# Optimization experiments

Measured on AMD Instinct MI355X. Metric: run time of the kernel, lower is better.

The kernel has to match this reference:

```python
import jax, jax.numpy as jnp
import numpy as np

SQRT_D = 16.0   # sqrt(d), d=256
BETA2 = 18.0    # beta^2 / 2, beta=6
EPS_BN = 1e-5


def _bn1d(x, g, b):
    # eval-mode BatchNorm1d with freshly-initialized running stats (mean=0, var=1)
    scale = g / jnp.sqrt(1.0 + EPS_BN)
    if x.ndim == 3:  # [B, C, N]
        return x * scale[:, None] + b[:, None]
    return x * scale + b  # [B, C]


def _crelu(z):
    return jax.nn.relu(z.real) + 1j * jax.nn.relu(z.imag)


def _sa_layer(x, qk_w, v_w, v_b, t_w, t_b, g, b):
    # x: [B, C, N]; q and k share weights (q_conv.weight = k_conv.weight)
    xq = jnp.einsum('oc,bcn->bno', qk_w, x)            # [B, N, C/4]
    xk = jnp.einsum('oc,bcn->bon', qk_w, x)            # [B, C/4, N]
    xv = jnp.einsum('oc,bcn->bon', v_w, x) + v_b[:, None]
    energy = jnp.einsum('bno,bom->bnm', xq, xk)        # [B, N, N]
    att = jax.nn.softmax(energy, axis=-1)
    att = att / (1e-9 + att.sum(axis=1, keepdims=True))  # sum-normalized over dim=1
    xr = jnp.einsum('bcn,bnm->bcm', xv, att)           # [B, C, N]
    xr = jax.nn.relu(_bn1d(jnp.einsum('oc,bcn->bon', t_w, x - xr) + t_b[:, None], g, b))
    return x + xr


def _forward(x, A, P, cl1_wr, cl1_wi, cl1_br, cl1_bi, cl2_wr, cl2_wi, cl2_br, cl2_bi,
             pt_conv1_w, pt_conv2_w, pt_bn1_g, pt_bn1_b, pt_bn2_g, pt_bn2_b,
             sa_qk_w, sa_v_w, sa_v_b, sa_t_w, sa_t_b, sa_bn_g, sa_bn_b,
             fuse_w, fuse_bn_g, fuse_bn_b, lin1_w, bn6_g, bn6_b,
             lin2_w, lin2_b, bn7_g, bn7_b, lin3_w, lin3_b):
    pts = jnp.transpose(x, (0, 2, 1))                  # [B, N, 3]
    # ---- VecKM: pairwise Gaussian kernel times complex random features ----
    sq = jnp.sum(pts * pts, axis=-1)                   # [B, N]
    D2 = sq[:, :, None] + sq[:, None, :] - 2.0 * jnp.einsum('bnc,bmc->bnm', pts, pts)
    J = jnp.exp(-BETA2 * D2).astype(jnp.complex64)     # [B, N, N]
    eA = jnp.exp(1j * (pts @ A))                       # [B, N, d] complex64
    G = (J @ eA) / eA
    G = G / jnp.linalg.norm(G, axis=-1, keepdims=True) * SQRT_D
    G = G + jnp.exp(1j * (pts @ P))                    # positional encoding
    # ---- ComplexLinear -> ComplexReLU -> ComplexLinear ----
    W1 = (cl1_wr + 1j * cl1_wi).astype(jnp.complex64)
    G = _crelu(G @ W1.T + (cl1_br + 1j * cl1_bi))
    W2 = (cl2_wr + 1j * cl2_wi).astype(jnp.complex64)
    G = G @ W2.T + (cl2_br + 1j * cl2_bi)
    Gr = G.real ** 2 + G.imag ** 2                     # [B, N, 256]
    Gc = jnp.transpose(Gr, (0, 2, 1))                  # [B, 256, N]
    # ---- Point_Transformer_Last ----
    h = jax.nn.relu(_bn1d(jnp.einsum('oc,bcn->bon', pt_conv1_w, Gc), pt_bn1_g, pt_bn1_b))
    h = jax.nn.relu(_bn1d(jnp.einsum('oc,bcn->bon', pt_conv2_w, h), pt_bn2_g, pt_bn2_b))
    feats = []
    for i in range(4):
        h = _sa_layer(h, sa_qk_w[i], sa_v_w[i], sa_v_b[i], sa_t_w[i], sa_t_b[i],
                      sa_bn_g[i], sa_bn_b[i])
        feats.append(h)
    h = jnp.concatenate(feats + [Gc], axis=1)          # [B, 1280, N]
    h = jax.nn.leaky_relu(_bn1d(jnp.einsum('oc,bcn->bon', fuse_w, h), fuse_bn_g, fuse_bn_b), 0.2)
    h = jnp.max(h, axis=-1)                            # adaptive_max_pool1d -> [B, 1024]
    h = jax.nn.leaky_relu(_bn1d(h @ lin1_w.T, bn6_g, bn6_b), 0.2)
    h = jax.nn.leaky_relu(_bn1d(h @ lin2_w.T + lin2_b, bn7_g, bn7_b), 0.2)
    return h @ lin3_w.T + lin3_b                       # [B, 40]


def setup_inputs() -> dict:
    key = jax.random.key(0)
    ks = iter(jax.random.split(key, 64))
    B, N, d = 16, 1024, 256
    r = lambda shape, s=0.05: jax.random.normal(next(ks), shape, dtype=jnp.float32) * s
    inp = {
        'x': jax.random.normal(next(ks), (B, 3, N), dtype=jnp.float32),
        'A': jax.random.normal(next(ks), (3, d), dtype=jnp.float32) * 30.0,
        'P': jax.random.normal(next(ks), (3, d), dtype=jnp.float32),
        'cl1_wr': r((d, d)), 'cl1_wi': r((d, d)), 'cl1_br': r((d,)), 'cl1_bi': r((d,)),
        'cl2_wr': r((d, d)), 'cl2_wi': r((d, d)), 'cl2_br': r((d,)), 'cl2_bi': r((d,)),
        'pt_conv1_w': r((256, 256)), 'pt_conv2_w': r((256, 256)),
        'pt_bn1_g': jnp.ones(256), 'pt_bn1_b': jnp.zeros(256),
        'pt_bn2_g': jnp.ones(256), 'pt_bn2_b': jnp.zeros(256),
        'sa_qk_w': r((4, 64, 256)), 'sa_v_w': r((4, 256, 256)), 'sa_v_b': r((4, 256)),
        'sa_t_w': r((4, 256, 256)), 'sa_t_b': r((4, 256)),
        'sa_bn_g': jnp.ones((4, 256)), 'sa_bn_b': jnp.zeros((4, 256)),
        'fuse_w': r((1024, 1280)), 'fuse_bn_g': jnp.ones(1024), 'fuse_bn_b': jnp.zeros(1024),
        'lin1_w': r((512, 1024)), 'bn6_g': jnp.ones(512), 'bn6_b': jnp.zeros(512),
        'lin2_w': r((256, 512)), 'lin2_b': r((256,)),
        'bn7_g': jnp.ones(256), 'bn7_b': jnp.zeros(256),
        'lin3_w': r((40, 256)), 'lin3_b': r((40,)),
    }
    return inp


def reference(x, A, P, cl1_wr, cl1_wi, cl1_br, cl1_bi, cl2_wr, cl2_wi, cl2_br, cl2_bi,
              pt_conv1_w, pt_conv2_w, pt_bn1_g, pt_bn1_b, pt_bn2_g, pt_bn2_b,
              sa_qk_w, sa_v_w, sa_v_b, sa_t_w, sa_t_b, sa_bn_g, sa_bn_b,
              fuse_w, fuse_bn_g, fuse_bn_b, lin1_w, bn6_g, bn6_b,
              lin2_w, lin2_b, bn7_g, bn7_b, lin3_w, lin3_b):
    return _forward(x, A, P, cl1_wr, cl1_wi, cl1_br, cl1_bi, cl2_wr, cl2_wi, cl2_br, cl2_bi,
                    pt_conv1_w, pt_conv2_w, pt_bn1_g, pt_bn1_b, pt_bn2_g, pt_bn2_b,
                    sa_qk_w, sa_v_w, sa_v_b, sa_t_w, sa_t_b, sa_bn_g, sa_bn_b,
                    fuse_w, fuse_bn_g, fuse_bn_b, lin1_w, bn6_g, bn6_b,
                    lin2_w, lin2_b, bn7_g, bn7_b, lin3_w, lin3_b)
```

## Files before the change

kernel.cpp:

```cpp
#include <hip/hip_runtime.h>
#include <math.h>

#define BB 16
#define NN 1024
#define DD 256

typedef unsigned short u16;
typedef unsigned int uint32;
typedef __attribute__((ext_vector_type(8))) short s8v;
typedef __attribute__((ext_vector_type(4))) float f4v;

__device__ __forceinline__ u16 f2b(float f) {
  uint32 u = __float_as_uint(f);
  return (u16)((u + 0x7fffu + ((u >> 16) & 1u)) >> 16);
}
__device__ __forceinline__ float b2f(u16 u) {
  return __uint_as_float(((uint32)u) << 16);
}

__device__ __forceinline__ float waveRedSum(float v) {
  #pragma unroll
  for (int o = 32; o; o >>= 1) v += __shfl_xor(v, o, 64);
  return v;
}
__device__ __forceinline__ float waveRedMax(float v) {
  #pragma unroll
  for (int o = 32; o; o >>= 1) v = fmaxf(v, __shfl_xor(v, o, 64));
  return v;
}

__global__ void k_pts(const float* __restrict__ x, float* __restrict__ pts) {
  int i = blockIdx.x * 256 + threadIdx.x;
  if (i >= BB * NN) return;
  int b = i >> 10, n = i & 1023;
  const float* xb = x + (size_t)b * 3 * NN;
  pts[i * 3 + 0] = xb[n];
  pts[i * 3 + 1] = xb[NN + n];
  pts[i * 3 + 2] = xb[2 * NN + n];
}

__global__ void k_phase(const float* __restrict__ pts, const float* __restrict__ A,
                        float2* __restrict__ eA) {
  int i = blockIdx.x * 256 + threadIdx.x;
  int d = i & 255; int bn = i >> 8;
  float p0 = pts[bn * 3], p1 = pts[bn * 3 + 1], p2 = pts[bn * 3 + 2];
  float ta = p0 * A[d] + p1 * A[256 + d] + p2 * A[512 + d];
  float s, c;
  sincosf(ta, &s, &c); eA[i] = make_float2(c, s);
}

__global__ void k_eat(const float2* __restrict__ eA, u16* __restrict__ eAT) {
  int bid = blockIdx.x;
  int dt = bid & 7, nt = (bid >> 3) & 15, b = bid >> 7;
  int d0 = dt * 32, n0 = nt * 64;
  __shared__ u16 cosT[32][72], sinT[32][72];
  int t = threadIdx.x;
  {
    int n = t >> 2, dg = (t & 3) * 8;
    const float2* p = eA + ((size_t)(b * 1024 + n0 + n)) * 256 + d0 + dg;
    #pragma unroll
    for (int j = 0; j < 8; j++) {
      float2 v = p[j];
      cosT[dg + j][n] = f2b(v.x);
      sinT[dg + j][n] = f2b(v.y);
    }
  }
  __syncthreads();
  {
    int rr = t >> 2, ng = (t & 3) * 16;
    int d = rr >> 1, cmp = rr & 1;
    const u16* src = (cmp ? &sinT[d][ng] : &cosT[d][ng]);
    uint4 v0 = *(const uint4*)src;
    uint4 v1 = *(const uint4*)(src + 8);
    u16* dst = eAT + ((size_t)(b * 512 + 2 * d0 + rr)) * 1024 + n0 + ng;
    *(uint4*)dst = v0;
    *(uint4*)(dst + 8) = v1;
  }
}

__global__ void k_jbuild(const float* __restrict__ pts, u16* __restrict__ J) {
  int bid = blockIdx.x;
  int b = bid >> 10, n = bid & 1023;
  int t = threadIdx.x;
  const float* pb = pts + (size_t)b * 3072;
  float pnx = pb[n * 3], pny = pb[n * 3 + 1], pnz = pb[n * 3 + 2];
  int m = t * 4;
  const float* pm = pb + (size_t)m * 3;
  float4 a = *(const float4*)pm;
  float4 bq = *(const float4*)(pm + 4);
  float4 c = *(const float4*)(pm + 8);
  float dx, dy, dz, d2;
  dx = a.x - pnx;  dy = a.y - pny;  dz = a.z - pnz;  d2 = dx*dx + dy*dy + dz*dz;
  float j0 = __expf(-18.0f * d2);
  dx = a.w - pnx;  dy = bq.x - pny; dz = bq.y - pnz; d2 = dx*dx + dy*dy + dz*dz;
  float j1 = __expf(-18.0f * d2);
  dx = bq.z - pnx; dy = bq.w - pny; dz = c.x - pnz;  d2 = dx*dx + dy*dy + dz*dz;
  float j2 = __expf(-18.0f * d2);
  dx = c.y - pnx;  dy = c.z - pny;  dz = c.w - pnz;  d2 = dx*dx + dy*dy + dz*dz;
  float j3 = __expf(-18.0f * d2);
  uint32 lo = (uint32)f2b(j0) | ((uint32)f2b(j1) << 16);
  uint32 hi = (uint32)f2b(j2) | ((uint32)f2b(j3) << 16);
  *(uint2*)(J + (size_t)bid * 1024 + m) = make_uint2(lo, hi);
}

__global__ void k_norm(const float2* __restrict__ M, const float2* __restrict__ eA,
                       const float* __restrict__ pts, const float* __restrict__ P,
                       u16* __restrict__ Gb) {
  int bn = blockIdx.x; int c = threadIdx.x;
  size_t idx = (size_t)bn * DD + c;
  float2 m = M[idx], e = eA[idx];
  float gr = m.x * e.x + m.y * e.y;
  float gi = m.y * e.x - m.x * e.y;
  float s = gr * gr + gi * gi;
  s = waveRedSum(s);
  __shared__ float red[4];
  if ((c & 63) == 0) red[c >> 6] = s;
  __syncthreads();
  float tot = red[0] + red[1] + red[2] + red[3];
  float scale = 16.0f / sqrtf(tot);
  float p0 = pts[bn * 3], p1 = pts[bn * 3 + 1], p2 = pts[bn * 3 + 2];
  float tp = p0 * P[c] + p1 * P[256 + c] + p2 * P[512 + c];
  float sp, cp; sincosf(tp, &sp, &cp);
  uint32 pk = (uint32)f2b(gr * scale + cp) | ((uint32)f2b(gi * scale + sp) << 16);
  *(uint32*)(Gb + idx * 2) = pk;
}

__global__ void k_cast(const float* __restrict__ s, u16* __restrict__ d, int n) {
  int i = blockIdx.x * 256 + threadIdx.x;
  if (i < n) d[i] = f2b(s[i]);
}
__global__ void k_wprep(const float* __restrict__ wr, const float* __restrict__ wi,
                        u16* __restrict__ dst) {
  int i = blockIdx.x * 256 + threadIdx.x;
  int op = i >> 9, c2 = i & 511, c = c2 >> 1, pl = c2 & 1;
  float v;
  if (op < 256) v = pl ? -wi[op * 256 + c] : wr[op * 256 + c];
  else          v = pl ?  wr[(op - 256) * 256 + c] : wi[(op - 256) * 256 + c];
  dst[i] = f2b(v);
}
__global__ void k_cbias(const float* __restrict__ br, const float* __restrict__ bi,
                        float* __restrict__ cb) {
  int t = threadIdx.x;
  cb[t] = (t < 256) ? br[t] : bi[t - 256];
}

__global__ void k_g2(const u16* __restrict__ G2b, u16* __restrict__ bigT) {
  int i = blockIdx.x * 256 + threadIdx.x;
  int row = i >> 8, c = i & 255;
  float re = b2f(G2b[(size_t)row * 512 + 2 * c]);
  float im = b2f(G2b[(size_t)row * 512 + 2 * c + 1]);
  bigT[(size_t)row * 1280 + 1024 + c] = f2b(re * re + im * im);
}

template<int BM>
__launch_bounds__(256)
__global__ void k_mm(const u16* __restrict__ Ab, long a_bs, int lda,
                     const u16* __restrict__ Btb, long b_bs, int ldb,
                     int K, int tiles_m, int tiles_n,
                     const float* __restrict__ bias,
                     const float* __restrict__ bng, const float* __restrict__ bnb,
                     const float* __restrict__ cbias,
                     int act,
                     const float* __restrict__ res, long res_bs, int res_sub,
                     float* __restrict__ outF, long outF_bs, int ldF,
                     u16* __restrict__ outB, long outB_bs, int ldBo, int ileave,
                     u16* __restrict__ outT, long outT_bs, int ldT) {
  constexpr int BN = 128;
  constexpr int WM = (BM == 128) ? 64 : 32;
  constexpr int MI = WM / 16;
  __shared__ u16 smem[BN * BM];
  u16* As = smem;
  u16* Bs = smem + BM * 32;
  int t = threadIdx.x;
  int l = t & 63, w = t >> 6;
  int p = l & 15, q = l >> 4;
  int bid = blockIdx.x;
  int tn = bid % tiles_n;
  int tm = (bid / tiles_n) % tiles_m;
  int b  = bid / (tiles_n * tiles_m);
  int m0 = tm * BM, n0 = tn * BN;
  int wm = w >> 1, wn = w & 1;
  const u16* Ap = Ab + (size_t)b * a_bs;
  const u16* Bp = Btb + (size_t)b * b_bs;

  f4v acc[MI][4];
  #pragma unroll
  for (int i = 0; i < MI; i++)
    #pragma unroll
    for (int j = 0; j < 4; j++) acc[i][j] = (f4v){0.f, 0.f, 0.f, 0.f};

  int arow = t >> 2, kg = (t & 3) * 8;
  for (int k0 = 0; k0 < K; k0 += 32) {
    __syncthreads();
    #pragma unroll
    for (int it = 0; it < BM / 64; it++) {
      int r = it * 64 + arow;
      float4 v = *(const float4*)(Ap + (size_t)(m0 + r) * lda + k0 + kg);
      *(float4*)&As[r * 32 + kg] = v;
    }
    #pragma unroll
    for (int it = 0; it < 2; it++) {
      int r = it * 64 + arow;
      float4 v = *(const float4*)(Bp + (size_t)(n0 + r) * ldb + k0 + kg);
      *(float4*)&Bs[r * 32 + kg] = v;
    }
    __syncthreads();
    s8v af[MI], bf[4];
    #pragma unroll
    for (int i = 0; i < MI; i++)
      af[i] = *(const s8v*)&As[(wm * WM + i * 16 + p) * 32 + q * 8];
    #pragma unroll
    for (int j = 0; j < 4; j++)
      bf[j] = *(const s8v*)&Bs[(wn * 64 + j * 16 + p) * 32 + q * 8];
    #pragma unroll
    for (int i = 0; i < MI; i++)
      #pragma unroll
      for (int j = 0; j < 4; j++)
        acc[i][j] = __builtin_amdgcn_mfma_f32_16x16x32_bf16(af[i], bf[j], acc[i][j], 0, 0, 0);
  }

  __syncthreads();

  float cbv[4];
  #pragma unroll
  for (int j = 0; j < 4; j++) {
    int no = n0 + wn * 64 + j * 16 + p;
    cbv[j] = cbias ? cbias[no] : 0.0f;
  }
  const float BNS = 0.99999500003749966f;
  #pragma unroll
  for (int i = 0; i < MI; i++) {
    #pragma unroll
    for (int r = 0; r < 4; r++) {
      int mo = m0 + wm * WM + i * 16 + q * 4 + r;
      float mult = 1.f, add = 0.f;
      if (bias) add = bias[mo];
      if (bng) { float s = bng[mo] * BNS; add = add * s + bnb[mo]; mult = s; }
      #pragma unroll
      for (int j = 0; j < 4; j++) {
        int no = n0 + wn * 64 + j * 16 + p;
        float v = acc[i][j][r];
        v = v * mult + add;
        if (cbias) v += cbv[j];
        if (act == 1) v = fmaxf(v, 0.f);
        else if (act == 2) v = v > 0.f ? v : 0.2f * v;
        if (res) {
          float rv = res[(size_t)b * res_bs + (size_t)mo * NN + no];
          v = res_sub ? rv - v : rv + v;
        }
        if (outF) outF[(size_t)b * outF_bs + (size_t)mo * ldF + no] = v;
        if (outB) {
          int noo = ileave ? (((no & 255) << 1) | (no >> 8)) : no;
          outB[(size_t)b * outB_bs + (size_t)mo * ldBo + noo] = f2b(v);
        }
        if (outT) smem[(wn * 64 + j * 16 + p) * BM + (mo - m0)] = f2b(v);
      }
    }
  }
  if (outT) {
    __syncthreads();
    constexpr int CPR = BM / 8;
    constexpr int RPP = 256 / CPR;
    int row0 = t / CPR, cg = (t % CPR) * 8;
    for (int rr = row0; rr < BN; rr += RPP) {
      float4 v = *(const float4*)&smem[rr * BM + cg];
      *(float4*)(outT + (size_t)b * outT_bs + (size_t)(n0 + rr) * ldT + m0 + cg) = v;
    }
  }
}

__global__ void k_rowstats(const float* __restrict__ E, float* __restrict__ rmax_,
                           float* __restrict__ rinv_) {
  int row = blockIdx.x;
  const float* pp = E + (size_t)row * NN;
  int t = threadIdx.x;
  float4 v = *(const float4*)(pp + t * 4);
  float mx = fmaxf(fmaxf(v.x, v.y), fmaxf(v.z, v.w));
  mx = waveRedMax(mx);
  __shared__ float redm[4];
  __shared__ float reds[4];
  if ((t & 63) == 0) redm[t >> 6] = mx;
  __syncthreads();
  mx = fmaxf(fmaxf(redm[0], redm[1]), fmaxf(redm[2], redm[3]));
  float s = __expf(v.x - mx) + __expf(v.y - mx) + __expf(v.z - mx) + __expf(v.w - mx);
  s = waveRedSum(s);
  if ((t & 63) == 0) reds[t >> 6] = s;
  __syncthreads();
  if (t == 0) {
    float tot = reds[0] + reds[1] + reds[2] + reds[3];
    rmax_[row] = mx;
    rinv_[row] = 1.0f / tot;
  }
}

__launch_bounds__(256)
__global__ void k_xratt(const u16* __restrict__ xv_, const float* __restrict__ E,
                        const float* __restrict__ rmax_, const float* __restrict__ rinv_,
                        const float* __restrict__ XinF, long xinF_bs,
                        u16* __restrict__ diffT) {
  __shared__ u16 smem[16384];
  __shared__ float colred[128][4];
  u16* As = smem;
  u16* Bs = smem + 4096;
  int t = threadIdx.x;
  int l = t & 63, w = t >> 6;
  int p = l & 15, q = l >> 4;
  int bid = blockIdx.x;
  int mt = bid & 7, ct = (bid >> 3) & 1, b = bid >> 4;
  int c0 = ct * 128, m0 = mt * 128;
  int wm = w >> 1, wn = w & 1;
  const u16* Ap = xv_ + (size_t)b * 262144;
  const float* Ep = E + ((size_t)b << 20);
  const float* rmx = rmax_ + (b << 10);
  const float* riv = rinv_ + (b << 10);
  f4v acc[4][4];
  #pragma unroll
  for (int i = 0; i < 4; i++)
    #pragma unroll
    for (int j = 0; j < 4; j++) acc[i][j] = (f4v){0.f, 0.f, 0.f, 0.f};
  float colpart0 = 0.f, colpart1 = 0.f;
  int arow = t >> 2, kg = (t & 3) * 8;
  for (int k0 = 0; k0 < 1024; k0 += 32) {
    __syncthreads();
    #pragma unroll
    for (int it = 0; it < 2; it++) {
      int r = it * 64 + arow;
      *(float4*)&As[r * 32 + kg] = *(const float4*)(Ap + (size_t)(c0 + r) * 1024 + k0 + kg);
    }
    float4 ma0 = *(const float4*)(rmx + k0 + kg);
    float4 ma1 = *(const float4*)(rmx + k0 + kg + 4);
    float4 ia0 = *(const float4*)(riv + k0 + kg);
    float4 ia1 = *(const float4*)(riv + k0 + kg + 4);
    #pragma unroll
    for (int it = 0; it < 2; it++) {
      int r = it * 64 + arow;
      const float* ep = Ep + (size_t)(m0 + r) * 1024 + k0 + kg;
      float4 e0 = *(const float4*)ep;
      float4 e1 = *(const float4*)(ep + 4);
      float p0 = __expf(e0.x - ma0.x) * ia0.x;
      float p1 = __expf(e0.y - ma0.y) * ia0.y;
      float p2 = __expf(e0.z - ma0.z) * ia0.z;
      float p3 = __expf(e0.w - ma0.w) * ia0.w;
      float p4 = __expf(e1.x - ma1.x) * ia1.x;
      float p5 = __expf(e1.y - ma1.y) * ia1.y;
      float p6 = __expf(e1.z - ma1.z) * ia1.z;
      float p7 = __expf(e1.w - ma1.w) * ia1.w;
      float s8 = ((p0 + p1) + (p2 + p3)) + ((p4 + p5) + (p6 + p7));
      if (it == 0) colpart0 += s8; else colpart1 += s8;
      uint32 w0 = (uint32)f2b(p0) | ((uint32)f2b(p1) << 16);
      uint32 w1 = (uint32)f2b(p2) | ((uint32)f2b(p3) << 16);
      uint32 w2 = (uint32)f2b(p4) | ((uint32)f2b(p5) << 16);
      uint32 w3 = (uint32)f2b(p6) | ((uint32)f2b(p7) << 16);
      *(uint4*)&Bs[r * 32 + kg] = make_uint4(w0, w1, w2, w3);
    }
    __syncthreads();
    s8v af[4], bf[4];
    #pragma unroll
    for (int i = 0; i < 4; i++)
      af[i] = *(const s8v*)&As[(wm * 64 + i * 16 + p) * 32 + q * 8];
    #pragma unroll
    for (int j = 0; j < 4; j++)
      bf[j] = *(const s8v*)&Bs[(wn * 64 + j * 16 + p) * 32 + q * 8];
    #pragma unroll
    for (int i = 0; i < 4; i++)
      #pragma unroll
      for (int j = 0; j < 4; j++)
        acc[i][j] = __builtin_amdgcn_mfma_f32_16x16x32_bf16(af[i], bf[j], acc[i][j], 0, 0, 0);
  }
  colred[arow][t & 3] = colpart0;
  colred[64 + arow][t & 3] = colpart1;
  __syncthreads();
  float csv[4];
  #pragma unroll
  for (int j = 0; j < 4; j++) {
    int ml = wn * 64 + j * 16 + p;
    csv[j] = 1.0f / (1e-9f + colred[ml][0] + colred[ml][1] + colred[ml][2] + colred[ml][3]);
  }
  #pragma unroll
  for (int i = 0; i < 4; i++) {
    #pragma unroll
    for (int r = 0; r < 4; r++) {
      int cl = wm * 64 + i * 16 + q * 4 + r;
      int c = c0 + cl;
      #pragma unroll
      for (int j = 0; j < 4; j++) {
        int ml = wn * 64 + j * 16 + p;
        float v = acc[i][j][r] * csv[j];
        float rv = XinF[(size_t)b * xinF_bs + (size_t)c * 1024 + m0 + ml];
        smem[ml * 128 + cl] = f2b(rv - v);
      }
    }
  }
  __syncthreads();
  int rr0 = t >> 4, cg = (t & 15) * 8;
  #pragma unroll
  for (int k = 0; k < 8; k++) {
    int rr = rr0 + k * 16;
    *(float4*)(diffT + (size_t)b * 262144 + (size_t)(m0 + rr) * 256 + c0 + cg) =
        *(const float4*)&smem[rr * 128 + cg];
  }
}

__global__ void k_maxpool(const float* __restrict__ fin, float* __restrict__ pool) {
  int bo = blockIdx.x;
  const float* pp = fin + (size_t)bo * NN;
  int t = threadIdx.x;
  float m = fmaxf(fmaxf(pp[t], pp[t + 256]), fmaxf(pp[t + 512], pp[t + 768]));
  m = waveRedMax(m);
  __shared__ float red[4];
  if ((t & 63) == 0) red[t >> 6] = m;
  __syncthreads();
  if (t == 0) pool[bo] = fmaxf(fmaxf(red[0], red[1]), fmaxf(red[2], red[3]));
}

__global__ void k_fc(const float* __restrict__ in, int Cc,
                     const float* __restrict__ W,
                     const float* __restrict__ bias,
                     const float* __restrict__ bng, const float* __restrict__ bnb,
                     int act, float* __restrict__ out, int O) {
  int i = blockIdx.x * 256 + threadIdx.x;
  if (i >= BB * O) return;
  int b = i / O, o = i % O;
  const float* xp = in + (size_t)b * Cc;
  const float* wp = W + (size_t)o * Cc;
  float s = 0.f;
  for (int c = 0; c < Cc; c += 4) {
    float4 xv = *(const float4*)(xp + c);
    float4 wv = *(const float4*)(wp + c);
    s += xv.x * wv.x + xv.y * wv.y + xv.z * wv.z + xv.w * wv.w;
  }
  if (bias) s += bias[o];
  const float BNS = 0.99999500003749966f;
  if (bng) s = s * (bng[o] * BNS) + bnb[o];
  if (act == 2) s = s > 0.f ? s : 0.2f * s;
  else if (act == 1) s = fmaxf(s, 0.f);
  out[i] = s;
}

extern "C" void kernel_launch(void* const* d_in, const int* in_sizes, int n_in,
                              void* d_out, int out_size, void* d_ws, size_t ws_size,
                              hipStream_t stream) {
  const float* x        = (const float*)d_in[0];
  const float* A        = (const float*)d_in[1];
  const float* P        = (const float*)d_in[2];
  const float* cl1_wr   = (const float*)d_in[3];
  const float* cl1_wi   = (const float*)d_in[4];
  const float* cl1_br   = (const float*)d_in[5];
  const float* cl1_bi   = (const float*)d_in[6];
  const float* cl2_wr   = (const float*)d_in[7];
  const float* cl2_wi   = (const float*)d_in[8];
  const float* cl2_br   = (const float*)d_in[9];
  const float* cl2_bi   = (const float*)d_in[10];
  const float* pt_c1_w  = (const float*)d_in[11];
  const float* pt_c2_w  = (const float*)d_in[12];
  const float* pt_bn1_g = (const float*)d_in[13];
  const float* pt_bn1_b = (const float*)d_in[14];
  const float* pt_bn2_g = (const float*)d_in[15];
  const float* pt_bn2_b = (const float*)d_in[16];
  const float* sa_qk_w  = (const float*)d_in[17];
  const float* sa_v_w   = (const float*)d_in[18];
  const float* sa_v_b   = (const float*)d_in[19];
  const float* sa_t_w   = (const float*)d_in[20];
  const float* sa_t_b   = (const float*)d_in[21];
  const float* sa_bn_g  = (const float*)d_in[22];
  const float* sa_bn_b  = (const float*)d_in[23];
  const float* fuse_w   = (const float*)d_in[24];
  const float* fuse_g   = (const float*)d_in[25];
  const float* fuse_b   = (const float*)d_in[26];
  const float* lin1_w   = (const float*)d_in[27];
  const float* bn6_g    = (const float*)d_in[28];
  const float* bn6_b    = (const float*)d_in[29];
  const float* lin2_w   = (const float*)d_in[30];
  const float* lin2_b   = (const float*)d_in[31];
  const float* bn7_g    = (const float*)d_in[32];
  const float* bn7_b    = (const float*)d_in[33];
  const float* lin3_w   = (const float*)d_in[34];
  const float* lin3_b   = (const float*)d_in[35];

  float* ws = (float*)d_ws;
  const size_t oPts  = 0;
  const size_t oS    = 65536;
  const size_t oBigT = oS + 16777216;
  const size_t oXf0  = oBigT + 10485760;
  const size_t oXf1  = oXf0 + 4194304;
  const size_t oH1T  = oXf1 + 4194304;
  const size_t oH2T  = oH1T + 2097152;
  const size_t oXkT  = oH2T + 2097152;
  const size_t oXv   = oXkT + 524288;
  const size_t oAux  = oXv + 2097152;
  const size_t oGb   = oAux + 8388608;
  const size_t oW1c  = oGb + 4194304;
  const size_t oW2c  = oW1c + 131072;
  const size_t oCb1  = oW2c + 131072;
  const size_t oCb2  = oCb1 + 512;
  const size_t oPool = oCb2 + 512;
  const size_t oFc1  = oPool + 16384;
  const size_t oFc2  = oFc1 + 8192;
  const size_t oWp   = oFc2 + 4096;

  float*  pts  = ws + oPts;
  float2* eA   = (float2*)(ws + oS);
  float2* Mj   = (float2*)(ws + oS + 8388608);
  u16*    G1b  = (u16*)(ws + oS);
  u16*    G2b  = (u16*)(ws + oS + 8388608);
  float*  Ebuf = ws + oS;
  float*  fuseO= ws + oS;
  u16*    bigT = (u16*)(ws + oBigT);
  float*  Xf0  = ws + oXf0;
  float*  Xf1  = ws + oXf1;
  u16*    h1T  = (u16*)(ws + oH1T);
  u16*    diffT= (u16*)(ws + oH1T);
  u16*    h2T  = (u16*)(ws + oH2T);
  u16*    xkT  = (u16*)(ws + oXkT);
  u16*    xv   = (u16*)(ws + oXv);
  u16*    eAT  = (u16*)(ws + oAux);
  u16*    Jb   = (u16*)(ws + oAux + 4194304);
  float*  rmax = ws + oAux;
  float*  rinv = ws + oAux + 16384;
  u16*    Gb   = (u16*)(ws + oGb);
  u16*    W1c  = (u16*)(ws + oW1c);
  u16*    W2c  = (u16*)(ws + oW2c);
  float*  cb1  = ws + oCb1;
  float*  cb2  = ws + oCb2;
  float*  pool = ws + oPool;
  float*  fc1  = ws + oFc1;
  float*  fc2  = ws + oFc2;
  u16*    wp   = (u16*)(ws + oWp);
  u16* wp_pt1  = wp;
  u16* wp_pt2  = wp + 65536;
  u16* wp_qk   = wp + 131072;
  u16* wp_v    = wp + 196608;
  u16* wp_t    = wp + 458752;
  u16* wp_fuse = wp + 720896;

  k_cast<<<256, 256, 0, stream>>>(pt_c1_w, wp_pt1, 65536);
  k_cast<<<256, 256, 0, stream>>>(pt_c2_w, wp_pt2, 65536);
  k_cast<<<256, 256, 0, stream>>>(sa_qk_w, wp_qk, 65536);
  k_cast<<<1024, 256, 0, stream>>>(sa_v_w, wp_v, 262144);
  k_cast<<<1024, 256, 0, stream>>>(sa_t_w, wp_t, 262144);
  k_cast<<<5120, 256, 0, stream>>>(fuse_w, wp_fuse, 1310720);
  k_wprep<<<1024, 256, 0, stream>>>(cl1_wr, cl1_wi, W1c);
  k_wprep<<<1024, 256, 0, stream>>>(cl2_wr, cl2_wi, W2c);
  k_cbias<<<1, 512, 0, stream>>>(cl1_br, cl1_bi, cb1);
  k_cbias<<<1, 512, 0, stream>>>(cl2_br, cl2_bi, cb2);

  k_pts<<<64, 256, 0, stream>>>(x, pts);
  k_phase<<<16384, 256, 0, stream>>>(pts, A, eA);
  k_eat<<<2048, 256, 0, stream>>>(eA, eAT);
  k_jbuild<<<16384, 256, 0, stream>>>(pts, Jb);
  k_mm<128><<<512, 256, 0, stream>>>(Jb, 1048576, 1024, eAT, 524288, 1024, 1024, 8, 4,
      nullptr, nullptr, nullptr, nullptr, 0, nullptr, 0, 0,
      (float*)Mj, 524288, 512, nullptr, 0, 0, 0, nullptr, 0, 0);
  k_norm<<<BB * NN, 256, 0, stream>>>(Mj, eA, pts, P, Gb);

  k_mm<128><<<512, 256, 0, stream>>>(Gb, 0, 512, W1c, 0, 512, 512, 128, 4,
      nullptr, nullptr, nullptr, cb1, 1, nullptr, 0, 0,
      nullptr, 0, 0, G1b, 0, 512, 1, nullptr, 0, 0);
  k_mm<128><<<512, 256, 0, stream>>>(G1b, 0, 512, W2c, 0, 512, 512, 128, 4,
      nullptr, nullptr, nullptr, cb2, 0, nullptr, 0, 0,
      nullptr, 0, 0, G2b, 0, 512, 1, nullptr, 0, 0);
  k_g2<<<16384, 256, 0, stream>>>(G2b, bigT);

  const long bsBigT = 1310720;
  const long bsH256 = 262144;
  const long bsXkT  = 65536;
  const long bsXvU  = 262144;
  const long bsF    = 262144;
  const long bsE    = 1048576;

  k_mm<128><<<256, 256, 0, stream>>>(wp_pt1, 0, 256, bigT + 1024, bsBigT, 1280, 256, 2, 8,
      nullptr, pt_bn1_g, pt_bn1_b, nullptr, 1, nullptr, 0, 0,
      nullptr, 0, 0, nullptr, 0, 0, 0, h1T, bsH256, 256);
  k_mm<128><<<256, 256, 0, stream>>>(wp_pt2, 0, 256, h1T, bsH256, 256, 256, 2, 8,
      nullptr, pt_bn2_g, pt_bn2_b, nullptr, 1, nullptr, 0, 0,
      Xf0, bsF, 1024, nullptr, 0, 0, 0, h2T, bsH256, 256);

  for (int i = 0; i < 4; i++) {
    const u16* XinT   = (i == 0) ? h2T : (bigT + (i - 1) * 256);
    long       xinT_bs= (i == 0) ? bsH256 : bsBigT;
    int        xinT_ld= (i == 0) ? 256 : 1280;
    float*     XinF   = (i & 1) ? Xf1 : Xf0;
    float*     XoutF  = (i & 1) ? Xf0 : Xf1;
    const u16* qkw = wp_qk + (size_t)i * 16384;
    const u16* vw  = wp_v + (size_t)i * 65536;
    const u16* tw  = wp_t + (size_t)i * 65536;

    k_mm<64><<<128, 256, 0, stream>>>(qkw, 0, 256, XinT, xinT_bs, xinT_ld, 256, 1, 8,
        nullptr, nullptr, nullptr, nullptr, 0, nullptr, 0, 0,
        nullptr, 0, 0, nullptr, 0, 0, 0, xkT, bsXkT, 64);
    k_mm<128><<<256, 256, 0, stream>>>(vw, 0, 256, XinT, xinT_bs, xinT_ld, 256, 2, 8,
        sa_v_b + i * 256, nullptr, nullptr, nullptr, 0, nullptr, 0, 0,
        nullptr, 0, 0, xv, bsXvU, 1024, 0, nullptr, 0, 0);
    k_mm<128><<<1024, 256, 0, stream>>>(xkT, bsXkT, 64, xkT, bsXkT, 64, 64, 8, 8,
        nullptr, nullptr, nullptr, nullptr, 0, nullptr, 0, 0,
        Ebuf, bsE, 1024, nullptr, 0, 0, 0, nullptr, 0, 0);
    k_rowstats<<<BB * NN, 256, 0, stream>>>(Ebuf, rmax, rinv);
    k_xratt<<<256, 256, 0, stream>>>(xv, Ebuf, rmax, rinv, XinF, bsF, diffT);
    k_mm<128><<<256, 256, 0, stream>>>(tw, 0, 256, diffT, bsH256, 256, 256, 2, 8,
        sa_t_b + i * 256, sa_bn_g + i * 256, sa_bn_b + i * 256, nullptr, 1,
        XinF, bsF, 0,
        XoutF, bsF, 1024, nullptr, 0, 0, 0, bigT + i * 256, bsBigT, 1280);
  }

  k_mm<128><<<1024, 256, 0, stream>>>(wp_fuse, 0, 1280, bigT, bsBigT, 1280, 1280, 8, 8,
      nullptr, fuse_g, fuse_b, nullptr, 2, nullptr, 0, 0,
      fuseO, 1048576, 1024, nullptr, 0, 0, 0, nullptr, 0, 0);
  k_maxpool<<<BB * 1024, 256, 0, stream>>>(fuseO, pool);

  k_fc<<<32, 256, 0, stream>>>(pool, 1024, lin1_w, nullptr, bn6_g, bn6_b, 2, fc1, 512);
  k_fc<<<16, 256, 0, stream>>>(fc1, 512, lin2_w, lin2_b, bn7_g, bn7_b, 2, fc2, 256);
  k_fc<<<3, 256, 0, stream>>>(fc2, 256, lin3_w, lin3_b, nullptr, nullptr, 0, (float*)d_out, 40);
}
```

Baseline: 1.096 ms.

## Store attention energies in bf16 and fuse max-pool into fuse GEMM epilogue

The attention energy matrix (B×N×N) is now written as bf16 instead of fp32, which halves the traffic in the energy GEMM store, the row-stats pass and the attention-apply kernel. The fuse GEMM no longer writes its full fp32 output. It reduces per-tile row maxima in its epilogue into a small partial buffer, and a tiny kernel finishes the max over the 8 column tiles. The cost is bf16 rounding of the softmax logits, which may affect accuracy.

```diff
diff --git a/kernel.cpp b/kernel.cpp
--- a/kernel.cpp
+++ b/kernel.cpp
@@ -17,6 +17,8 @@
 __device__ __forceinline__ float b2f(u16 u) {
   return __uint_as_float(((uint32)u) << 16);
 }
+__device__ __forceinline__ float blo(uint32 w) { return __uint_as_float(w << 16); }
+__device__ __forceinline__ float bhi(uint32 w) { return __uint_as_float(w & 0xffff0000u); }
 
 __device__ __forceinline__ float waveRedSum(float v) {
   #pragma unroll
@@ -164,7 +166,8 @@
                      const float* __restrict__ res, long res_bs, int res_sub,
                      float* __restrict__ outF, long outF_bs, int ldF,
                      u16* __restrict__ outB, long outB_bs, int ldBo, int ileave,
-                     u16* __restrict__ outT, long outT_bs, int ldT) {
+                     u16* __restrict__ outT, long outT_bs, int ldT,
+                     float* __restrict__ outPool) {
   constexpr int BN = 128;
   constexpr int WM = (BM == 128) ? 64 : 32;
   constexpr int MI = WM / 16;
@@ -227,6 +230,11 @@
     int no = n0 + wn * 64 + j * 16 + p;
     cbv[j] = cbias ? cbias[no] : 0.0f;
   }
+  float pmax[MI][4];
+  #pragma unroll
+  for (int i = 0; i < MI; i++)
+    #pragma unroll
+    for (int r = 0; r < 4; r++) pmax[i][r] = -3.0e38f;
   const float BNS = 0.99999500003749966f;
   #pragma unroll
   for (int i = 0; i < MI; i++) {
@@ -248,6 +256,7 @@
           float rv = res[(size_t)b * res_bs + (size_t)mo * NN + no];
           v = res_sub ? rv - v : rv + v;
         }
+        if (outPool) pmax[i][r] = fmaxf(pmax[i][r], v);
         if (outF) outF[(size_t)b * outF_bs + (size_t)mo * ldF + no] = v;
         if (outB) {
           int noo = ileave ? (((no & 255) << 1) | (no >> 8)) : no;
@@ -267,22 +276,40 @@
       *(float4*)(outT + (size_t)b * outT_bs + (size_t)(n0 + rr) * ldT + m0 + cg) = v;
     }
   }
-}
-
-__global__ void k_rowstats(const float* __restrict__ E, float* __restrict__ rmax_,
+  if (outPool) {
+    float* pf = (float*)smem;
+    #pragma unroll
+    for (int i = 0; i < MI; i++)
+      #pragma unroll
+      for (int r = 0; r < 4; r++) {
+        float m = pmax[i][r];
+        #pragma unroll
+        for (int o = 1; o < 16; o <<= 1) m = fmaxf(m, __shfl_xor(m, o, 64));
+        if (p == 0) pf[(wm * WM + i * 16 + q * 4 + r) * 2 + wn] = m;
+      }
+    __syncthreads();
+    if (t < BM) {
+      float mv = fmaxf(pf[t * 2], pf[t * 2 + 1]);
+      outPool[((size_t)b * (tiles_m * BM) + m0 + t) * tiles_n + tn] = mv;
+    }
+  }
+}
+
+__global__ void k_rowstats(const u16* __restrict__ E, float* __restrict__ rmax_,
                            float* __restrict__ rinv_) {
   int row = blockIdx.x;
-  const float* pp = E + (size_t)row * NN;
+  const u16* pp = E + (size_t)row * NN;
   int t = threadIdx.x;
-  float4 v = *(const float4*)(pp + t * 4);
-  float mx = fmaxf(fmaxf(v.x, v.y), fmaxf(v.z, v.w));
+  uint2 wv = *(const uint2*)(pp + t * 4);
+  float v0 = blo(wv.x), v1 = bhi(wv.x), v2 = blo(wv.y), v3 = bhi(wv.y);
+  float mx = fmaxf(fmaxf(v0, v1), fmaxf(v2, v3));
   mx = waveRedMax(mx);
   __shared__ float redm[4];
   __shared__ float reds[4];
   if ((t & 63) == 0) redm[t >> 6] = mx;
   __syncthreads();
   mx = fmaxf(fmaxf(redm[0], redm[1]), fmaxf(redm[2], redm[3]));
-  float s = __expf(v.x - mx) + __expf(v.y - mx) + __expf(v.z - mx) + __expf(v.w - mx);
+  float s = __expf(v0 - mx) + __expf(v1 - mx) + __expf(v2 - mx) + __expf(v3 - mx);
   s = waveRedSum(s);
   if ((t & 63) == 0) reds[t >> 6] = s;
   __syncthreads();
@@ -294,7 +321,7 @@
 }
 
 __launch_bounds__(256)
-__global__ void k_xratt(const u16* __restrict__ xv_, const float* __restrict__ E,
+__global__ void k_xratt(const u16* __restrict__ xv_, const u16* __restrict__ E,
                         const float* __restrict__ rmax_, const float* __restrict__ rinv_,
                         const float* __restrict__ XinF, long xinF_bs,
                         u16* __restrict__ diffT) {
@@ -310,7 +337,7 @@
   int c0 = ct * 128, m0 = mt * 128;
   int wm = w >> 1, wn = w & 1;
   const u16* Ap = xv_ + (size_t)b * 262144;
-  const float* Ep = E + ((size_t)b << 20);
+  const u16* Ep = E + ((size_t)b << 20);
   const float* rmx = rmax_ + (b << 10);
   const float* riv = rinv_ + (b << 10);
   f4v acc[4][4];
@@ -334,17 +361,15 @@
     #pragma unroll
     for (int it = 0; it < 2; it++) {
       int r = it * 64 + arow;
-      const float* ep = Ep + (size_t)(m0 + r) * 1024 + k0 + kg;
-      float4 e0 = *(const float4*)ep;
-      float4 e1 = *(const float4*)(ep + 4);
-      float p0 = __expf(e0.x - ma0.x) * ia0.x;
-      float p1 = __expf(e0.y - ma0.y) * ia0.y;
-      float p2 = __expf(e0.z - ma0.z) * ia0.z;
-      float p3 = __expf(e0.w - ma0.w) * ia0.w;
-      float p4 = __expf(e1.x - ma1.x) * ia1.x;
-      float p5 = __expf(e1.y - ma1.y) * ia1.y;
-      float p6 = __expf(e1.z - ma1.z) * ia1.z;
-      float p7 = __expf(e1.w - ma1.w) * ia1.w;
+      uint4 e8 = *(const uint4*)(Ep + (size_t)(m0 + r) * 1024 + k0 + kg);
+      float p0 = __expf(blo(e8.x) - ma0.x) * ia0.x;
+      float p1 = __expf(bhi(e8.x) - ma0.y) * ia0.y;
+      float p2 = __expf(blo(e8.y) - ma0.z) * ia0.z;
+      float p3 = __expf(bhi(e8.y) - ma0.w) * ia0.w;
+      float p4 = __expf(blo(e8.z) - ma1.x) * ia1.x;
+      float p5 = __expf(bhi(e8.z) - ma1.y) * ia1.y;
+      float p6 = __expf(blo(e8.w) - ma1.z) * ia1.z;
+      float p7 = __expf(bhi(e8.w) - ma1.w) * ia1.w;
       float s8 = ((p0 + p1) + (p2 + p3)) + ((p4 + p5) + (p6 + p7));
       if (it == 0) colpart0 += s8; else colpart1 += s8;
       uint32 w0 = (uint32)f2b(p0) | ((uint32)f2b(p1) << 16);
@@ -401,16 +426,12 @@
   }
 }
 
-__global__ void k_maxpool(const float* __restrict__ fin, float* __restrict__ pool) {
-  int bo = blockIdx.x;
-  const float* pp = fin + (size_t)bo * NN;
-  int t = threadIdx.x;
-  float m = fmaxf(fmaxf(pp[t], pp[t + 256]), fmaxf(pp[t + 512], pp[t + 768]));
-  m = waveRedMax(m);
-  __shared__ float red[4];
-  if ((t & 63) == 0) red[t >> 6] = m;
-  __syncthreads();
-  if (t == 0) pool[bo] = fmaxf(fmaxf(red[0], red[1]), fmaxf(red[2], red[3]));
+__global__ void k_pool8(const float* __restrict__ pp, float* __restrict__ pool) {
+  int i = blockIdx.x * 256 + threadIdx.x;
+  const float4* p4 = (const float4*)(pp + (size_t)i * 8);
+  float4 a = p4[0], b = p4[1];
+  pool[i] = fmaxf(fmaxf(fmaxf(a.x, a.y), fmaxf(a.z, a.w)),
+                  fmaxf(fmaxf(b.x, b.y), fmaxf(b.z, b.w)));
 }
 
 __global__ void k_fc(const float* __restrict__ in, int Cc,
@@ -503,8 +524,8 @@
   float2* Mj   = (float2*)(ws + oS + 8388608);
   u16*    G1b  = (u16*)(ws + oS);
   u16*    G2b  = (u16*)(ws + oS + 8388608);
-  float*  Ebuf = ws + oS;
-  float*  fuseO= ws + oS;
+  u16*    Eb   = (u16*)(ws + oS);
+  float*  poolP= ws + oS + 8388608;
   u16*    bigT = (u16*)(ws + oBigT);
   float*  Xf0  = ws + oXf0;
   float*  Xf1  = ws + oXf1;
@@ -550,15 +571,15 @@
   k_jbuild<<<16384, 256, 0, stream>>>(pts, Jb);
   k_mm<128><<<512, 256, 0, stream>>>(Jb, 1048576, 1024, eAT, 524288, 1024, 1024, 8, 4,
       nullptr, nullptr, nullptr, nullptr, 0, nullptr, 0, 0,
-      (float*)Mj, 524288, 512, nullptr, 0, 0, 0, nullptr, 0, 0);
+      (float*)Mj, 524288, 512, nullptr, 0, 0, 0, nullptr, 0, 0, nullptr);
   k_norm<<<BB * NN, 256, 0, stream>>>(Mj, eA, pts, P, Gb);
 
   k_mm<128><<<512, 256, 0, stream>>>(Gb, 0, 512, W1c, 0, 512, 512, 128, 4,
       nullptr, nullptr, nullptr, cb1, 1, nullptr, 0, 0,
-      nullptr, 0, 0, G1b, 0, 512, 1, nullptr, 0, 0);
+      nullptr, 0, 0, G1b, 0, 512, 1, nullptr, 0, 0, nullptr);
   k_mm<128><<<512, 256, 0, stream>>>(G1b, 0, 512, W2c, 0, 512, 512, 128, 4,
       nullptr, nullptr, nullptr, cb2, 0, nullptr, 0, 0,
-      nullptr, 0, 0, G2b, 0, 512, 1, nullptr, 0, 0);
+      nullptr, 0, 0, G2b, 0, 512, 1, nullptr, 0, 0, nullptr);
   k_g2<<<16384, 256, 0, stream>>>(G2b, bigT);
 
   const long bsBigT = 1310720;
@@ -566,14 +587,14 @@
   const long bsXkT  = 65536;
   const long bsXvU  = 262144;
   const long bsF    = 262144;
-  const long bsE    = 1048576;
+  const long bsEU   = 1048576;
 
   k_mm<128><<<256, 256, 0, stream>>>(wp_pt1, 0, 256, bigT + 1024, bsBigT, 1280, 256, 2, 8,
       nullptr, pt_bn1_g, pt_bn1_b, nullptr, 1, nullptr, 0, 0,
-      nullptr, 0, 0, nullptr, 0, 0, 0, h1T, bsH256, 256);
+      nullptr, 0, 0, nullptr, 0, 0, 0, h1T, bsH256, 256, nullptr);
   k_mm<128><<<256, 256, 0, stream>>>(wp_pt2, 0, 256, h1T, bsH256, 256, 256, 2, 8,
       nullptr, pt_bn2_g, pt_bn2_b, nullptr, 1, nullptr, 0, 0,
-      Xf0, bsF, 1024, nullptr, 0, 0, 0, h2T, bsH256, 256);
+      Xf0, bsF, 1024, nullptr, 0, 0, 0, h2T, bsH256, 256, nullptr);
 
   for (int i = 0; i < 4; i++) {
     const u16* XinT   = (i == 0) ? h2T : (bigT + (i - 1) * 256);
@@ -587,25 +608,25 @@
 
     k_mm<64><<<128, 256, 0, stream>>>(qkw, 0, 256, XinT, xinT_bs, xinT_ld, 256, 1, 8,
         nullptr, nullptr, nullptr, nullptr, 0, nullptr, 0, 0,
-        nullptr, 0, 0, nullptr, 0, 0, 0, xkT, bsXkT, 64);
+        nullptr, 0, 0, nullptr, 0, 0, 0, xkT, bsXkT, 64, nullptr);
     k_mm<128><<<256, 256, 0, stream>>>(vw, 0, 256, XinT, xinT_bs, xinT_ld, 256, 2, 8,
         sa_v_b + i * 256, nullptr, nullptr, nullptr, 0, nullptr, 0, 0,
-        nullptr, 0, 0, xv, bsXvU, 1024, 0, nullptr, 0, 0);
+        nullptr, 0, 0, xv, bsXvU, 1024, 0, nullptr, 0, 0, nullptr);
     k_mm<128><<<1024, 256, 0, stream>>>(xkT, bsXkT, 64, xkT, bsXkT, 64, 64, 8, 8,
         nullptr, nullptr, nullptr, nullptr, 0, nullptr, 0, 0,
-        Ebuf, bsE, 1024, nullptr, 0, 0, 0, nullptr, 0, 0);
-    k_rowstats<<<BB * NN, 256, 0, stream>>>(Ebuf, rmax, rinv);
-    k_xratt<<<256, 256, 0, stream>>>(xv, Ebuf, rmax, rinv, XinF, bsF, diffT);
+        nullptr, 0, 0, Eb, bsEU, 1024, 0, nullptr, 0, 0, nullptr);
+    k_rowstats<<<BB * NN, 256, 0, stream>>>(Eb, rmax, rinv);
+    k_xratt<<<256, 256, 0, stream>>>(xv, Eb, rmax, rinv, XinF, bsF, diffT);
     k_mm<128><<<256, 256, 0, stream>>>(tw, 0, 256, diffT, bsH256, 256, 256, 2, 8,
         sa_t_b + i * 256, sa_bn_g + i * 256, sa_bn_b + i * 256, nullptr, 1,
         XinF, bsF, 0,
-        XoutF, bsF, 1024, nullptr, 0, 0, 0, bigT + i * 256, bsBigT, 1280);
+        XoutF, bsF, 1024, nullptr, 0, 0, 0, bigT + i * 256, bsBigT, 1280, nullptr);
   }
 
   k_mm<128><<<1024, 256, 0, stream>>>(wp_fuse, 0, 1280, bigT, bsBigT, 1280, 1280, 8, 8,
       nullptr, fuse_g, fuse_b, nullptr, 2, nullptr, 0, 0,
-      fuseO, 1048576, 1024, nullptr, 0, 0, 0, nullptr, 0, 0);
-  k_maxpool<<<BB * 1024, 256, 0, stream>>>(fuseO, pool);
+      nullptr, 0, 0, nullptr, 0, 0, 0, nullptr, 0, 0, poolP);
+  k_pool8<<<64, 256, 0, stream>>>(poolP, pool);
 
   k_fc<<<32, 256, 0, stream>>>(pool, 1024, lin1_w, nullptr, bn6_g, bn6_b, 2, fc1, 512);
   k_fc<<<16, 256, 0, stream>>>(fc1, 512, lin2_w, lin2_b, bn7_g, bn7_b, 2, fc2, 256);
```

Result: no change. 1.105 ms (+0.8%).
